# Kernel tuning notes

Measured on AMD Instinct MI355X. Metric: run time of the kernel, lower is better.

## Reference

```python
import jax, jax.numpy as jnp
import numpy as np

N, E, H = 50000, 800000, 4

def setup_inputs() -> dict:
    key = jax.random.key(0)
    ks = jax.random.split(key, 16)
    feat = jax.random.normal(ks[0], (N, 2), dtype=jnp.float32)
    src = jax.random.randint(ks[1], (E,), 0, N, dtype=jnp.int32)
    dst = jax.random.randint(ks[2], (E,), 0, N, dtype=jnp.int32)
    def w(k, shape, fan_in):
        return jax.random.normal(k, shape, dtype=jnp.float32) * (1.0 / np.sqrt(fan_in))
    # layer 1: 2 -> 4 heads x 32
    W1 = w(ks[3], (2, 128), 2); al1 = w(ks[4], (H, 32), 32); ar1 = w(ks[5], (H, 32), 32); b1 = jnp.zeros((128,), jnp.float32)
    # layer 2: 128 -> 4 heads x 32
    W2 = w(ks[6], (128, 128), 128); al2 = w(ks[7], (H, 32), 32); ar2 = w(ks[8], (H, 32), 32); b2 = jnp.zeros((128,), jnp.float32)
    # layer 3: 128 -> 4 heads x 64
    W3 = w(ks[9], (128, 256), 128); al3 = w(ks[10], (H, 64), 64); ar3 = w(ks[11], (H, 64), 64); b3 = jnp.zeros((256,), jnp.float32)
    return dict(feat=feat, src=src, dst=dst, W1=W1, al1=al1, ar1=ar1, b1=b1,
                W2=W2, al2=al2, ar2=ar2, b2=b2, W3=W3, al3=al3, ar3=ar3, b3=b3)

def gat_layer(h, W, al, ar, b, src, dst):
    # h: [N, Fin]; W: [Fin, H*D]; al/ar: [H, D]; b: [H*D]
    Hh, D = al.shape
    z = (h @ W).reshape(-1, Hh, D)                      # [N, H, D]
    el = jnp.sum(z * al[None], axis=-1)                 # [N, H]
    er = jnp.sum(z * ar[None], axis=-1)                 # [N, H]
    e = jax.nn.leaky_relu(el[src] + er[dst], 0.2)       # [E, H]
    m = jax.ops.segment_max(e, dst, num_segments=N)     # [N, H] per-dst max
    ex = jnp.exp(e - m[dst])                            # [E, H]
    s = jax.ops.segment_sum(ex, dst, num_segments=N)    # [N, H]
    alpha = ex / s[dst]                                 # edge softmax
    msg = z[src] * alpha[:, :, None]                    # [E, H, D] gathered+weighted
    out = jax.ops.segment_sum(msg, dst, num_segments=N) # [N, H, D]
    return out.reshape(N, Hh * D) + b

def reference(feat, src, dst, W1, al1, ar1, b1, W2, al2, ar2, b2, W3, al3, ar3, b3):
    # dropout is identity at inference
    h = jax.nn.relu(gat_layer(feat, W1, al1, ar1, b1, src, dst))
    h = jax.nn.relu(gat_layer(h, W2, al2, ar2, b2, src, dst))
    h = gat_layer(h, W3, al3, ar3, b3, src, dst)
    return h
```

## Files before the change

### kernel.cpp

```cpp
#include <hip/hip_runtime.h>
#include <math.h>


#define NEG_BIG (-1e38f)

typedef _Float16 h8 __attribute__((ext_vector_type(8)));
typedef _Float16 h4 __attribute__((ext_vector_type(4)));
typedef float f32x4 __attribute__((ext_vector_type(4)));

static inline int cdiv(int a, int b) { return (a + b - 1) / b; }

__device__ __forceinline__ float lrelu(float x) { return (x >= 0.f) ? x : 0.2f * x; }


__global__ void count_deg_kernel(const int* __restrict__ dst, int* __restrict__ deg, int E) {
    int i = blockIdx.x * blockDim.x + threadIdx.x;
    if (i < E) atomicAdd(&deg[dst[i]], 1);
}

__global__ __launch_bounds__(256) void scan1_kernel(const int* __restrict__ deg,
                                                    int* __restrict__ rowptr,
                                                    int* __restrict__ bsum, int n) {
    __shared__ int wsum[4];
    int t = threadIdx.x;
    int l = t & 63, wv = t >> 6;
    int i = blockIdx.x * 256 + t;
    int v = (i < n) ? deg[i] : 0;
    int x = v;
    #pragma unroll
    for (int off = 1; off < 64; off <<= 1) {
        int y = __shfl_up(x, off);
        if (l >= off) x += y;
    }
    if (l == 63) wsum[wv] = x;
    __syncthreads();
    int wo = 0;
    #pragma unroll
    for (int j = 0; j < 4; ++j)
        if (j < wv) wo += wsum[j];
    if (i < n) rowptr[i] = wo + x - v;
    if (t == 255) bsum[blockIdx.x] = wo + x;
}

__global__ __launch_bounds__(256) void scan2_kernel(const int* __restrict__ bsum,
                                                    int* __restrict__ boff, int nb) {
    __shared__ int wsum[4];
    int t = threadIdx.x;
    int l = t & 63, wv = t >> 6;
    int v = (t < nb) ? bsum[t] : 0;
    int x = v;
    #pragma unroll
    for (int off = 1; off < 64; off <<= 1) {
        int y = __shfl_up(x, off);
        if (l >= off) x += y;
    }
    if (l == 63) wsum[wv] = x;
    __syncthreads();
    int wo = 0;
    #pragma unroll
    for (int j = 0; j < 4; ++j)
        if (j < wv) wo += wsum[j];
    if (t < nb) boff[t] = wo + x - v;
}

__global__ __launch_bounds__(256) void scan3_kernel(int* __restrict__ rowptr,
                                                    const int* __restrict__ boff,
                                                    int n, int E) {
    int i = blockIdx.x * 256 + threadIdx.x;
    if (i < n) rowptr[i] += boff[blockIdx.x];
    if (i == 0) rowptr[n] = E;
}

__global__ void fill_csr_kernel(const int* __restrict__ src, const int* __restrict__ dst,
                                const int* __restrict__ rowptr,
                                int* __restrict__ cursor, int* __restrict__ csrc, int E) {
    int i = blockIdx.x * blockDim.x + threadIdx.x;
    if (i < E) {
        int d = dst[i];
        int pos = atomicAdd(&cursor[d], 1);
        csrc[rowptr[d] + pos] = src[i];
    }
}


template <int HDOUT>
__global__ __launch_bounds__(256) void wconv_kernel(const float* __restrict__ W,
                                                    _Float16* __restrict__ WT) {
    int idx = blockIdx.x * 256 + threadIdx.x;
    if (idx < 128 * HDOUT) {
        int k = idx / HDOUT, c = idx % HDOUT;
        WT[(size_t)c * 128 + k] = (_Float16)W[idx];
    }
}


__global__ __launch_bounds__(256) void agg1_kernel(
        const float* __restrict__ feat, const float* __restrict__ W1,
        const float* __restrict__ al, const float* __restrict__ ar,
        const int* __restrict__ rowptr, const int* __restrict__ csrc,
        const float* __restrict__ bias, _Float16* __restrict__ out, int N) {
    constexpr int GRP = 16, NV = 4;
    __shared__ float2 fss[4][NV][GRP + 1];
    __shared__ float  exs[4][NV][4][GRP + 1];
    const int l = threadIdx.x & 63;
    const int w = threadIdx.x >> 6;
    const int g = l >> 4;
    const int lg = l & 15;
    const int v = blockIdx.x * (4 * NV) + w * NV + g;

    float w0l = W1[l], w0h = W1[l + 64];
    float w1l = W1[128 + l], w1h = W1[128 + l + 64];
    float all_ = al[l], alh = al[l + 64];
    float arl = ar[l], arh = ar[l + 64];
    float pa0 = w0l * all_, pa1 = w0h * alh;
    float pb0 = w1l * all_, pb1 = w1h * alh;
    float pc0 = w0l * arl,  pc1 = w0h * arh;
    float pd0 = w1l * arl,  pd1 = w1h * arh;
    #pragma unroll
    for (int off = 1; off < 32; off <<= 1) {
        pa0 += __shfl_xor(pa0, off); pa1 += __shfl_xor(pa1, off);
        pb0 += __shfl_xor(pb0, off); pb1 += __shfl_xor(pb1, off);
        pc0 += __shfl_xor(pc0, off); pc1 += __shfl_xor(pc1, off);
        pd0 += __shfl_xor(pd0, off); pd1 += __shfl_xor(pd1, off);
    }
    float4 Ael = make_float4(__shfl(pa0, 0), __shfl(pa0, 32),
                             __shfl(pa1, 0), __shfl(pa1, 32));
    float4 Bel = make_float4(__shfl(pb0, 0), __shfl(pb0, 32),
                             __shfl(pb1, 0), __shfl(pb1, 32));
    float4 Aer = make_float4(__shfl(pc0, 0), __shfl(pc0, 32),
                             __shfl(pc1, 0), __shfl(pc1, 32));
    float4 Ber = make_float4(__shfl(pd0, 0), __shfl(pd0, 32),
                             __shfl(pd1, 0), __shfl(pd1, 32));

    if (v >= N) return;
    const int r0 = rowptr[v], r1 = rowptr[v + 1];
    const int c0 = lg * 8;
    const int h = lg >> 2;
    float4 w0a = *(const float4*)&W1[c0];
    float4 w0b = *(const float4*)&W1[c0 + 4];
    float4 w1a = *(const float4*)&W1[128 + c0];
    float4 w1b = *(const float4*)&W1[128 + c0 + 4];
    float4 b0 = *(const float4*)(bias + c0);
    float4 b1 = *(const float4*)(bias + c0 + 4);
    float4 o0, o1;

    if (r0 == r1) {
        o0 = b0; o1 = b1;
    } else {
        float2 fv = *(const float2*)(feat + (size_t)v * 2);
        float4 er4 = make_float4(fmaf(fv.x, Aer.x, fv.y * Ber.x),
                                 fmaf(fv.x, Aer.y, fv.y * Ber.y),
                                 fmaf(fv.x, Aer.z, fv.y * Ber.z),
                                 fmaf(fv.x, Aer.w, fv.y * Ber.w));

        float m0 = NEG_BIG, m1 = NEG_BIG, m2 = NEG_BIG, m3 = NEG_BIG;
        float2 fs0 = make_float2(0.f, 0.f);
        float4 e40 = make_float4(NEG_BIG, NEG_BIG, NEG_BIG, NEG_BIG);
        for (int base = r0; base < r1; base += GRP) {
            int i = base + lg;
            float ex_ = NEG_BIG, ey_ = NEG_BIG, ez_ = NEG_BIG, ew_ = NEG_BIG;
            float2 fs = make_float2(0.f, 0.f);
            if (i < r1) {
                int sv = csrc[i];
                fs = *(const float2*)(feat + (size_t)sv * 2);
                ex_ = lrelu(fmaf(fs.x, Ael.x, fs.y * Bel.x) + er4.x);
                ey_ = lrelu(fmaf(fs.x, Ael.y, fs.y * Bel.y) + er4.y);
                ez_ = lrelu(fmaf(fs.x, Ael.z, fs.y * Bel.z) + er4.z);
                ew_ = lrelu(fmaf(fs.x, Ael.w, fs.y * Bel.w) + er4.w);
            }
            if (base == r0) { fs0 = fs; e40 = make_float4(ex_, ey_, ez_, ew_); }
            m0 = fmaxf(m0, ex_); m1 = fmaxf(m1, ey_);
            m2 = fmaxf(m2, ez_); m3 = fmaxf(m3, ew_);
        }
        #pragma unroll
        for (int off = 1; off < GRP; off <<= 1) {
            m0 = fmaxf(m0, __shfl_xor(m0, off));
            m1 = fmaxf(m1, __shfl_xor(m1, off));
            m2 = fmaxf(m2, __shfl_xor(m2, off));
            m3 = fmaxf(m3, __shfl_xor(m3, off));
        }

        float s0 = 0.f, s1 = 0.f, s2 = 0.f, s3 = 0.f;
        float4 a0 = make_float4(0.f, 0.f, 0.f, 0.f);
        float4 a1 = make_float4(0.f, 0.f, 0.f, 0.f);

        for (int base = r0; base < r1; base += GRP) {
            int i = base + lg;
            float2 fs; float4 e4;
            if (base == r0) {
                fs = fs0; e4 = e40;
            } else if (i < r1) {
                int sv = csrc[i];
                fs = *(const float2*)(feat + (size_t)sv * 2);
                e4 = make_float4(
                    lrelu(fmaf(fs.x, Ael.x, fs.y * Bel.x) + er4.x),
                    lrelu(fmaf(fs.x, Ael.y, fs.y * Bel.y) + er4.y),
                    lrelu(fmaf(fs.x, Ael.z, fs.y * Bel.z) + er4.z),
                    lrelu(fmaf(fs.x, Ael.w, fs.y * Bel.w) + er4.w));
            } else {
                fs = make_float2(0.f, 0.f);
                e4 = make_float4(NEG_BIG, NEG_BIG, NEG_BIG, NEG_BIG);
            }
            bool valid = (i < r1);
            float exv0 = valid ? __expf(e4.x - m0) : 0.f;
            float exv1 = valid ? __expf(e4.y - m1) : 0.f;
            float exv2 = valid ? __expf(e4.z - m2) : 0.f;
            float exv3 = valid ? __expf(e4.w - m3) : 0.f;
            s0 += exv0; s1 += exv1; s2 += exv2; s3 += exv3;
            fss[w][g][lg] = fs;
            exs[w][g][0][lg] = exv0; exs[w][g][1][lg] = exv1;
            exs[w][g][2][lg] = exv2; exs[w][g][3][lg] = exv3;
            int cnt = min(GRP, r1 - base);
            #pragma unroll 8
            for (int k = 0; k < cnt; ++k) {
                float2 fk = fss[w][g][k];
                float exk = exs[w][g][h][k];
                float u = fk.x * exk;
                float t = fk.y * exk;
                a0.x = fmaf(u, w0a.x, fmaf(t, w1a.x, a0.x));
                a0.y = fmaf(u, w0a.y, fmaf(t, w1a.y, a0.y));
                a0.z = fmaf(u, w0a.z, fmaf(t, w1a.z, a0.z));
                a0.w = fmaf(u, w0a.w, fmaf(t, w1a.w, a0.w));
                a1.x = fmaf(u, w0b.x, fmaf(t, w1b.x, a1.x));
                a1.y = fmaf(u, w0b.y, fmaf(t, w1b.y, a1.y));
                a1.z = fmaf(u, w0b.z, fmaf(t, w1b.z, a1.z));
                a1.w = fmaf(u, w0b.w, fmaf(t, w1b.w, a1.w));
            }
        }
        #pragma unroll
        for (int off = 1; off < GRP; off <<= 1) {
            s0 += __shfl_xor(s0, off);
            s1 += __shfl_xor(s1, off);
            s2 += __shfl_xor(s2, off);
            s3 += __shfl_xor(s3, off);
        }
        float s = (h == 0) ? s0 : (h == 1) ? s1 : (h == 2) ? s2 : s3;
        float inv = 1.f / s;
        o0 = make_float4(fmaf(a0.x, inv, b0.x), fmaf(a0.y, inv, b0.y),
                         fmaf(a0.z, inv, b0.z), fmaf(a0.w, inv, b0.w));
        o1 = make_float4(fmaf(a1.x, inv, b1.x), fmaf(a1.y, inv, b1.y),
                         fmaf(a1.z, inv, b1.z), fmaf(a1.w, inv, b1.w));
    }
    o0.x = fmaxf(o0.x, 0.f); o0.y = fmaxf(o0.y, 0.f);
    o0.z = fmaxf(o0.z, 0.f); o0.w = fmaxf(o0.w, 0.f);
    o1.x = fmaxf(o1.x, 0.f); o1.y = fmaxf(o1.y, 0.f);
    o1.z = fmaxf(o1.z, 0.f); o1.w = fmaxf(o1.w, 0.f);
    h8 ho;
    ho[0] = (_Float16)o0.x; ho[1] = (_Float16)o0.y;
    ho[2] = (_Float16)o0.z; ho[3] = (_Float16)o0.w;
    ho[4] = (_Float16)o1.x; ho[5] = (_Float16)o1.y;
    ho[6] = (_Float16)o1.z; ho[7] = (_Float16)o1.w;
    *(h8*)(out + (size_t)v * 128 + c0) = ho;
}


template <int HDOUT>
__global__ __launch_bounds__(256) void gemm_mfma_kernel(
        const _Float16* __restrict__ A, const _Float16* __restrict__ WT,
        const float* __restrict__ al, const float* __restrict__ ar,
        _Float16* __restrict__ ZH, float* __restrict__ el, float* __restrict__ er,
        int N) {
    constexpr int TPH = HDOUT / 64;
    const int l = threadIdx.x & 63;
    const int wid = blockIdx.x * 4 + (threadIdx.x >> 6);
    const int m0 = wid * 16;
    if (m0 >= N) return;
    const int lc = l & 15;
    const int kg = l >> 4;

    h8 afrag[4];
    {
        int m = m0 + lc;
        if (m < N) {
            const _Float16* ap = A + (size_t)m * 128 + kg * 8;
            #pragma unroll
            for (int ks = 0; ks < 4; ++ks) afrag[ks] = *(const h8*)(ap + ks * 32);
        } else {
            #pragma unroll
            for (int ks = 0; ks < 4; ++ks)
                #pragma unroll
                for (int j = 0; j < 8; ++j) afrag[ks][j] = (_Float16)0.f;
        }
    }

    #pragma unroll
    for (int h = 0; h < 4; ++h) {
        float pel[4] = {0.f, 0.f, 0.f, 0.f};
        float per_[4] = {0.f, 0.f, 0.f, 0.f};
        #pragma unroll
        for (int tt = 0; tt < TPH; ++tt) {
            int col = (h * TPH + tt) * 16 + lc;
            f32x4 acc = {0.f, 0.f, 0.f, 0.f};
            const _Float16* wp = WT + (size_t)col * 128 + kg * 8;
            #pragma unroll
            for (int ks = 0; ks < 4; ++ks) {
                h8 bfrag = *(const h8*)(wp + ks * 32);
                acc = __builtin_amdgcn_mfma_f32_16x16x32_f16(afrag[ks], bfrag, acc,
                                                             0, 0, 0);
            }
            float alc = al[col], arc = ar[col];
            #pragma unroll
            for (int r = 0; r < 4; ++r) {
                int n = m0 + kg * 4 + r;
                if (n < N) ZH[(size_t)n * HDOUT + col] = (_Float16)acc[r];
                pel[r] = fmaf(acc[r], alc, pel[r]);
                per_[r] = fmaf(acc[r], arc, per_[r]);
            }
        }
        #pragma unroll
        for (int off = 1; off < 16; off <<= 1) {
            #pragma unroll
            for (int r = 0; r < 4; ++r) {
                pel[r] += __shfl_xor(pel[r], off);
                per_[r] += __shfl_xor(per_[r], off);
            }
        }
        if (lc == 0) {
            #pragma unroll
            for (int r = 0; r < 4; ++r) {
                int n = m0 + kg * 4 + r;
                if (n < N) {
                    el[(size_t)n * 4 + h] = pel[r];
                    er[(size_t)n * 4 + h] = per_[r];
                }
            }
        }
    }
}


template <bool RELU, int GRP, int HD, typename OUTT>
__global__ __launch_bounds__(256) void agg_kernel(
        const _Float16* __restrict__ zh, const float* __restrict__ el,
        const float* __restrict__ er, const int* __restrict__ rowptr,
        const int* __restrict__ csrc, const float* __restrict__ bias,
        OUTT* __restrict__ out, int N) {
    constexpr int NV = 64 / GRP;
    constexpr int CH = HD / GRP;
    constexpr int HGRP = GRP / 4;
    static_assert(CH == 8, "config assumes 8 channels per lane");
    __shared__ float exs[4][NV][4][GRP + 1];
    __shared__ int   svs[4][NV][GRP + 1];
    const int l = threadIdx.x & 63;
    const int w = threadIdx.x >> 6;
    const int g = l / GRP;
    const int lg = l & (GRP - 1);
    const int v = blockIdx.x * (4 * NV) + w * NV + g;
    if (v >= N) return;
    const int r0 = rowptr[v], r1 = rowptr[v + 1];
    const int c0 = lg * CH;
    const int h = lg / HGRP;
    float4 b0 = *(const float4*)(bias + c0);
    float4 b1 = *(const float4*)(bias + c0 + 4);
    float4 o0, o1;

    if (r0 == r1) {
        o0 = b0; o1 = b1;
    } else {
        float4 er4 = *(const float4*)(er + (size_t)v * 4);

        float m0 = NEG_BIG, m1 = NEG_BIG, m2 = NEG_BIG, m3 = NEG_BIG;
        int sv0 = 0;
        float4 e40 = make_float4(NEG_BIG, NEG_BIG, NEG_BIG, NEG_BIG);
        for (int base = r0; base < r1; base += GRP) {
            int i = base + lg;
            float ex_ = NEG_BIG, ey_ = NEG_BIG, ez_ = NEG_BIG, ew_ = NEG_BIG;
            int sv = 0;
            if (i < r1) {
                sv = csrc[i];
                float4 ev = *(const float4*)(el + (size_t)sv * 4);
                ex_ = lrelu(ev.x + er4.x);
                ey_ = lrelu(ev.y + er4.y);
                ez_ = lrelu(ev.z + er4.z);
                ew_ = lrelu(ev.w + er4.w);
            }
            if (base == r0) { sv0 = sv; e40 = make_float4(ex_, ey_, ez_, ew_); }
            m0 = fmaxf(m0, ex_); m1 = fmaxf(m1, ey_);
            m2 = fmaxf(m2, ez_); m3 = fmaxf(m3, ew_);
        }
        #pragma unroll
        for (int off = 1; off < GRP; off <<= 1) {
            m0 = fmaxf(m0, __shfl_xor(m0, off));
            m1 = fmaxf(m1, __shfl_xor(m1, off));
            m2 = fmaxf(m2, __shfl_xor(m2, off));
            m3 = fmaxf(m3, __shfl_xor(m3, off));
        }

        float s0 = 0.f, s1 = 0.f, s2 = 0.f, s3 = 0.f;
        float4 a0 = make_float4(0.f, 0.f, 0.f, 0.f);
        float4 a1 = make_float4(0.f, 0.f, 0.f, 0.f);

        for (int base = r0; base < r1; base += GRP) {
            int i = base + lg;
            int sv; float4 e4;
            if (base == r0) {
                sv = sv0; e4 = e40;
            } else if (i < r1) {
                sv = csrc[i];
                float4 ev = *(const float4*)(el + (size_t)sv * 4);
                e4 = make_float4(lrelu(ev.x + er4.x), lrelu(ev.y + er4.y),
                                 lrelu(ev.z + er4.z), lrelu(ev.w + er4.w));
            } else {
                sv = 0; e4 = make_float4(NEG_BIG, NEG_BIG, NEG_BIG, NEG_BIG);
            }
            bool valid = (i < r1);
            float exv0 = valid ? __expf(e4.x - m0) : 0.f;
            float exv1 = valid ? __expf(e4.y - m1) : 0.f;
            float exv2 = valid ? __expf(e4.z - m2) : 0.f;
            float exv3 = valid ? __expf(e4.w - m3) : 0.f;
            s0 += exv0; s1 += exv1; s2 += exv2; s3 += exv3;
            svs[w][g][lg] = sv;
            exs[w][g][0][lg] = exv0; exs[w][g][1][lg] = exv1;
            exs[w][g][2][lg] = exv2; exs[w][g][3][lg] = exv3;
            int cnt = min(GRP, r1 - base);
            #pragma unroll 8
            for (int k = 0; k < cnt; ++k) {
                int svk = svs[w][g][k];
                float exk = exs[w][g][h][k];
                h8 zz = *(const h8*)(zh + (size_t)svk * HD + c0);
                a0.x = fmaf((float)zz[0], exk, a0.x);
                a0.y = fmaf((float)zz[1], exk, a0.y);
                a0.z = fmaf((float)zz[2], exk, a0.z);
                a0.w = fmaf((float)zz[3], exk, a0.w);
                a1.x = fmaf((float)zz[4], exk, a1.x);
                a1.y = fmaf((float)zz[5], exk, a1.y);
                a1.z = fmaf((float)zz[6], exk, a1.z);
                a1.w = fmaf((float)zz[7], exk, a1.w);
            }
        }
        #pragma unroll
        for (int off = 1; off < GRP; off <<= 1) {
            s0 += __shfl_xor(s0, off);
            s1 += __shfl_xor(s1, off);
            s2 += __shfl_xor(s2, off);
            s3 += __shfl_xor(s3, off);
        }
        float s = (h == 0) ? s0 : (h == 1) ? s1 : (h == 2) ? s2 : s3;
        float inv = 1.f / s;
        o0 = make_float4(fmaf(a0.x, inv, b0.x), fmaf(a0.y, inv, b0.y),
                         fmaf(a0.z, inv, b0.z), fmaf(a0.w, inv, b0.w));
        o1 = make_float4(fmaf(a1.x, inv, b1.x), fmaf(a1.y, inv, b1.y),
                         fmaf(a1.z, inv, b1.z), fmaf(a1.w, inv, b1.w));
    }
    if (RELU) {
        o0.x = fmaxf(o0.x, 0.f); o0.y = fmaxf(o0.y, 0.f);
        o0.z = fmaxf(o0.z, 0.f); o0.w = fmaxf(o0.w, 0.f);
        o1.x = fmaxf(o1.x, 0.f); o1.y = fmaxf(o1.y, 0.f);
        o1.z = fmaxf(o1.z, 0.f); o1.w = fmaxf(o1.w, 0.f);
    }
    if constexpr (sizeof(OUTT) == 2) {
        h8 ho;
        ho[0] = (_Float16)o0.x; ho[1] = (_Float16)o0.y;
        ho[2] = (_Float16)o0.z; ho[3] = (_Float16)o0.w;
        ho[4] = (_Float16)o1.x; ho[5] = (_Float16)o1.y;
        ho[6] = (_Float16)o1.z; ho[7] = (_Float16)o1.w;
        *(h8*)((_Float16*)out + (size_t)v * HD + c0) = ho;
    } else {
        float* op = (float*)out + (size_t)v * HD + c0;
        *(float4*)op = o0;
        *(float4*)(op + 4) = o1;
    }
}


extern "C" void kernel_launch(void* const* d_in, const int* in_sizes, int n_in,
                              void* d_out, int out_size, void* d_ws, size_t ws_size,
                              hipStream_t stream) {
    const float* feat = (const float*)d_in[0];
    const int* src = (const int*)d_in[1];
    const int* dst = (const int*)d_in[2];
    const float* W1 = (const float*)d_in[3];
    const float* al1 = (const float*)d_in[4];
    const float* ar1 = (const float*)d_in[5];
    const float* b1 = (const float*)d_in[6];
    const float* W2 = (const float*)d_in[7];
    const float* al2 = (const float*)d_in[8];
    const float* ar2 = (const float*)d_in[9];
    const float* b2 = (const float*)d_in[10];
    const float* W3 = (const float*)d_in[11];
    const float* al3 = (const float*)d_in[12];
    const float* ar3 = (const float*)d_in[13];
    const float* b3 = (const float*)d_in[14];
    const int N = in_sizes[0] / 2;
    const int E = in_sizes[1];

    _Float16* hbuf = (_Float16*)d_ws;
    float* el = (float*)(hbuf + (size_t)N * 128);
    float* er = el + (size_t)N * 4;
    _Float16* zh = (_Float16*)(er + (size_t)N * 4);
    _Float16* WT2 = zh + (size_t)N * 256;
    _Float16* WT3 = WT2 + 128 * 128;
    int* csrc = (int*)(WT3 + 256 * 128);
    int* deg = csrc + E;
    int* cursor = deg + N;
    int* rowptr = cursor + N;
    int* bsum = rowptr + (N + 1);
    int* boff = bsum + 256;

    const int nb = cdiv(N, 256);

    hipMemsetAsync(deg, 0, sizeof(int) * (size_t)(2 * N), stream);
    wconv_kernel<128><<<cdiv(128 * 128, 256), 256, 0, stream>>>(W2, WT2);
    wconv_kernel<256><<<cdiv(128 * 256, 256), 256, 0, stream>>>(W3, WT3);
    count_deg_kernel<<<cdiv(E, 256), 256, 0, stream>>>(dst, deg, E);
    scan1_kernel<<<nb, 256, 0, stream>>>(deg, rowptr, bsum, N);
    scan2_kernel<<<1, 256, 0, stream>>>(bsum, boff, nb);
    scan3_kernel<<<nb, 256, 0, stream>>>(rowptr, boff, N, E);
    fill_csr_kernel<<<cdiv(E, 256), 256, 0, stream>>>(src, dst, rowptr, cursor, csrc, E);

    agg1_kernel<<<cdiv(N, 16), 256, 0, stream>>>(feat, W1, al1, ar1, rowptr, csrc,
                                                 b1, hbuf, N);

    gemm_mfma_kernel<128><<<cdiv(N, 64), 256, 0, stream>>>(
        hbuf, WT2, al2, ar2, zh, el, er, N);
    agg_kernel<true, 16, 128, _Float16><<<cdiv(N, 16), 256, 0, stream>>>(
        zh, el, er, rowptr, csrc, b2, hbuf, N);

    gemm_mfma_kernel<256><<<cdiv(N, 64), 256, 0, stream>>>(
        hbuf, WT3, al3, ar3, zh, el, er, N);
    agg_kernel<false, 32, 256, float><<<cdiv(N, 8), 256, 0, stream>>>(
        zh, el, er, rowptr, csrc, b3, (float*)d_out, N);
}
```

Baseline: 291.5 us.

## Trim preprocessing launches, vectorize CSR build, stage GEMM output through LDS

Merges the two weight-conversion kernels into one launch. The scan2 and scan3 kernels are replaced by a single kernel in which each block sums the preceding block totals itself. The degree-count and CSR-fill kernels now handle four edges per thread using int4 loads. The MFMA GEMM writes its Z tile to shared memory first, then stores it to global memory as coalesced 16-byte rows instead of scattered 2-byte stores. This removes launch overhead and uncoalesced writes, at the cost of extra LDS use per block in the GEMM.

```diff
diff --git a/kernel.cpp b/kernel.cpp
--- a/kernel.cpp
+++ b/kernel.cpp
@@ -14,8 +14,16 @@
 
 
 __global__ void count_deg_kernel(const int* __restrict__ dst, int* __restrict__ deg, int E) {
-    int i = blockIdx.x * blockDim.x + threadIdx.x;
-    if (i < E) atomicAdd(&deg[dst[i]], 1);
+    int i = (blockIdx.x * blockDim.x + threadIdx.x) * 4;
+    if (i + 3 < E) {
+        int4 d = *(const int4*)(dst + i);
+        atomicAdd(&deg[d.x], 1);
+        atomicAdd(&deg[d.y], 1);
+        atomicAdd(&deg[d.z], 1);
+        atomicAdd(&deg[d.w], 1);
+    } else {
+        for (int j = i; j < E; ++j) atomicAdd(&deg[dst[j]], 1);
+    }
 }
 
 __global__ __launch_bounds__(256) void scan1_kernel(const int* __restrict__ deg,
@@ -42,54 +50,58 @@
     if (t == 255) bsum[blockIdx.x] = wo + x;
 }
 
-__global__ __launch_bounds__(256) void scan2_kernel(const int* __restrict__ bsum,
-                                                    int* __restrict__ boff, int nb) {
+__global__ __launch_bounds__(256) void scan3_kernel(int* __restrict__ rowptr,
+                                                    const int* __restrict__ bsum,
+                                                    int n, int E, int nb) {
     __shared__ int wsum[4];
     int t = threadIdx.x;
     int l = t & 63, wv = t >> 6;
-    int v = (t < nb) ? bsum[t] : 0;
-    int x = v;
+    int bi = blockIdx.x;
+    int v = (t < bi) ? bsum[t] : 0;
     #pragma unroll
-    for (int off = 1; off < 64; off <<= 1) {
-        int y = __shfl_up(x, off);
-        if (l >= off) x += y;
-    }
-    if (l == 63) wsum[wv] = x;
+    for (int off = 1; off < 64; off <<= 1) v += __shfl_xor(v, off);
+    if (l == 0) wsum[wv] = v;
     __syncthreads();
-    int wo = 0;
-    #pragma unroll
-    for (int j = 0; j < 4; ++j)
-        if (j < wv) wo += wsum[j];
-    if (t < nb) boff[t] = wo + x - v;
-}
-
-__global__ __launch_bounds__(256) void scan3_kernel(int* __restrict__ rowptr,
-                                                    const int* __restrict__ boff,
-                                                    int n, int E) {
-    int i = blockIdx.x * 256 + threadIdx.x;
-    if (i < n) rowptr[i] += boff[blockIdx.x];
+    int off = wsum[0] + wsum[1] + wsum[2] + wsum[3];
+    int i = bi * 256 + t;
+    if (i < n) rowptr[i] += off;
     if (i == 0) rowptr[n] = E;
 }
 
 __global__ void fill_csr_kernel(const int* __restrict__ src, const int* __restrict__ dst,
                                 const int* __restrict__ rowptr,
                                 int* __restrict__ cursor, int* __restrict__ csrc, int E) {
-    int i = blockIdx.x * blockDim.x + threadIdx.x;
-    if (i < E) {
-        int d = dst[i];
-        int pos = atomicAdd(&cursor[d], 1);
-        csrc[rowptr[d] + pos] = src[i];
-    }
-}
-
-
-template <int HDOUT>
-__global__ __launch_bounds__(256) void wconv_kernel(const float* __restrict__ W,
-                                                    _Float16* __restrict__ WT) {
+    int i = (blockIdx.x * blockDim.x + threadIdx.x) * 4;
+    if (i + 3 < E) {
+        int4 d = *(const int4*)(dst + i);
+        int4 s = *(const int4*)(src + i);
+        int p;
+        p = atomicAdd(&cursor[d.x], 1); csrc[rowptr[d.x] + p] = s.x;
+        p = atomicAdd(&cursor[d.y], 1); csrc[rowptr[d.y] + p] = s.y;
+        p = atomicAdd(&cursor[d.z], 1); csrc[rowptr[d.z] + p] = s.z;
+        p = atomicAdd(&cursor[d.w], 1); csrc[rowptr[d.w] + p] = s.w;
+    } else {
+        for (int j = i; j < E; ++j) {
+            int dd = dst[j];
+            int p = atomicAdd(&cursor[dd], 1);
+            csrc[rowptr[dd] + p] = src[j];
+        }
+    }
+}
+
+
+__global__ __launch_bounds__(256) void wconv_kernel(const float* __restrict__ W2,
+                                                    const float* __restrict__ W3,
+                                                    _Float16* __restrict__ WT2,
+                                                    _Float16* __restrict__ WT3) {
     int idx = blockIdx.x * 256 + threadIdx.x;
-    if (idx < 128 * HDOUT) {
-        int k = idx / HDOUT, c = idx % HDOUT;
-        WT[(size_t)c * 128 + k] = (_Float16)W[idx];
+    if (idx < 128 * 128) {
+        int k = idx >> 7, c = idx & 127;
+        WT2[(size_t)c * 128 + k] = (_Float16)W2[idx];
+    } else if (idx < 128 * 128 + 128 * 256) {
+        int j = idx - 128 * 128;
+        int k = j >> 8, c = j & 255;
+        WT3[(size_t)c * 128 + k] = (_Float16)W3[j];
     }
 }
 
@@ -261,8 +273,10 @@
         _Float16* __restrict__ ZH, float* __restrict__ el, float* __restrict__ er,
         int N) {
     constexpr int TPH = HDOUT / 64;
+    __shared__ _Float16 zst[4][16][HDOUT];
     const int l = threadIdx.x & 63;
-    const int wid = blockIdx.x * 4 + (threadIdx.x >> 6);
+    const int w = threadIdx.x >> 6;
+    const int wid = blockIdx.x * 4 + w;
     const int m0 = wid * 16;
     if (m0 >= N) return;
     const int lc = l & 15;
@@ -301,8 +315,7 @@
             float alc = al[col], arc = ar[col];
             #pragma unroll
             for (int r = 0; r < 4; ++r) {
-                int n = m0 + kg * 4 + r;
-                if (n < N) ZH[(size_t)n * HDOUT + col] = (_Float16)acc[r];
+                zst[w][kg * 4 + r][col] = (_Float16)acc[r];
                 pel[r] = fmaf(acc[r], alc, pel[r]);
                 per_[r] = fmaf(acc[r], arc, per_[r]);
             }
@@ -325,6 +338,16 @@
                 }
             }
         }
+    }
+
+    #pragma unroll
+    for (int it = 0; it < HDOUT / 32; ++it) {
+        int idx = (it * 64 + l) * 8;
+        int r = idx / HDOUT;
+        int c = idx % HDOUT;
+        int n = m0 + r;
+        if (n < N)
+            *(h8*)&ZH[(size_t)n * HDOUT + c] = *(const h8*)&zst[w][r][c];
     }
 }
 
@@ -495,18 +518,15 @@
     int* cursor = deg + N;
     int* rowptr = cursor + N;
     int* bsum = rowptr + (N + 1);
-    int* boff = bsum + 256;
 
     const int nb = cdiv(N, 256);
 
     hipMemsetAsync(deg, 0, sizeof(int) * (size_t)(2 * N), stream);
-    wconv_kernel<128><<<cdiv(128 * 128, 256), 256, 0, stream>>>(W2, WT2);
-    wconv_kernel<256><<<cdiv(128 * 256, 256), 256, 0, stream>>>(W3, WT3);
-    count_deg_kernel<<<cdiv(E, 256), 256, 0, stream>>>(dst, deg, E);
+    wconv_kernel<<<cdiv(128 * 128 + 128 * 256, 256), 256, 0, stream>>>(W2, W3, WT2, WT3);
+    count_deg_kernel<<<cdiv(E, 1024), 256, 0, stream>>>(dst, deg, E);
     scan1_kernel<<<nb, 256, 0, stream>>>(deg, rowptr, bsum, N);
-    scan2_kernel<<<1, 256, 0, stream>>>(bsum, boff, nb);
-    scan3_kernel<<<nb, 256, 0, stream>>>(rowptr, boff, N, E);
-    fill_csr_kernel<<<cdiv(E, 256), 256, 0, stream>>>(src, dst, rowptr, cursor, csrc, E);
+    scan3_kernel<<<nb, 256, 0, stream>>>(rowptr, bsum, N, E, nb);
+    fill_csr_kernel<<<cdiv(E, 1024), 256, 0, stream>>>(src, dst, rowptr, cursor, csrc, E);
 
     agg1_kernel<<<cdiv(N, 16), 256, 0, stream>>>(feat, W1, al1, ar1, rowptr, csrc,
                                                  b1, hbuf, N);
```

After: 290.5 us. Within noise of the previous version (-0.3%).
